# Kernel tuning notes

Measured on AMD Instinct MI355X. Metric: run time of the kernel, lower is better.

## Reference

```python
import jax, jax.numpy as jnp
import numpy as np

DECAY = 0.99
EPS = 1e-05


def setup_inputs() -> dict:
    key = jax.random.key(0)
    k1, k2 = jax.random.split(key)
    B, C, H, W = 64, 256, 32, 32
    n_embed = 1024
    inp = jax.random.normal(k1, (B, C, H, W), dtype=jnp.float32)
    embed = jax.random.normal(k2, (C, n_embed), dtype=jnp.float32)
    cluster_size = jnp.ones((n_embed,), dtype=jnp.float32)
    embed_avg = embed.copy()
    return {"input": inp, "embed": embed, "cluster_size": cluster_size, "embed_avg": embed_avg}


def reference(input, embed, cluster_size, embed_avg):
    n_embed = embed.shape[1]
    x = jnp.transpose(input, (0, 2, 3, 1))            # B,H,W,C
    flatten = x.reshape(-1, x.shape[-1])              # N,C
    dist = ((flatten ** 2).sum(1, keepdims=True)
            - 2.0 * flatten @ embed
            + (embed ** 2).sum(0, keepdims=True))     # N,n_embed
    embed_ind = jnp.argmin(dist, axis=1)              # N
    quantize = jnp.take(embed.T, embed_ind, axis=0).reshape(x.shape)  # B,H,W,C
    embed_ind_out = embed_ind.reshape(x.shape[:-1])   # B,H,W

    # EMA codebook update (training=True)
    onehot_sum = jnp.zeros((n_embed,), dtype=flatten.dtype).at[embed_ind].add(1.0)
    embed_sum = jax.ops.segment_sum(flatten, embed_ind, num_segments=n_embed).T  # C,n_embed
    cluster_size_new = cluster_size * DECAY + onehot_sum * (1.0 - DECAY)
    embed_avg_new = embed_avg * DECAY + embed_sum * (1.0 - DECAY)
    n = cluster_size_new.sum()
    cs = (cluster_size_new + EPS) / (n + n_embed * EPS) * n
    embed_new = embed_avg_new / cs[None, :]

    diff = jax.lax.stop_gradient(quantize) - x
    quantize_st = x + jax.lax.stop_gradient(quantize - x)   # straight-through
    quantize_out = jnp.transpose(quantize_st, (0, 3, 1, 2)) # B,C,H,W
    return quantize_out, diff, embed_ind_out, embed_new, cluster_size_new, embed_avg_new
```

## Files before the change

kernel.cpp:

```cpp
#include <hip/hip_runtime.h>
#include <cstddef>

static constexpr int OUT_DIFF = 16777216;
static constexpr int OUT_IDX  = 33554432;
static constexpr int OUT_ENEW = 33619968;
static constexpr int OUT_CSN  = 33882112;
static constexpr int OUT_EAVG = 33883136;

__global__ __launch_bounds__(256) void k_prep(const float* __restrict__ embed,
                                              const float* __restrict__ cs_in,
                                              float* __restrict__ embedT,
                                              float* __restrict__ esq,
                                              float* __restrict__ nval) {
  const int wg = blockIdx.x;
  const int tid = threadIdx.x;
  if (wg < 1024) {
    __shared__ float col[256];
    const int k = wg;
    float v = embed[(size_t)tid * 1024 + k];
    col[tid] = v;
    embedT[(size_t)k * 256 + tid] = v;
    __syncthreads();
    if (tid == 0) {
#pragma clang fp contract(off)
      float s = 0.f;
      for (int c = 0; c < 256; ++c) { float u = col[c]; s += u * u; }
      esq[k] = s;
    }
  } else {
    __shared__ float red[256];
    float v = cs_in[tid] + cs_in[tid + 256] + cs_in[tid + 512] + cs_in[tid + 768];
    red[tid] = v;
    __syncthreads();
    for (int off = 128; off > 0; off >>= 1) {
      if (tid < off) red[tid] += red[tid + off];
      __syncthreads();
    }
    if (tid == 0) nval[0] = 0.99f * red[0] + 0.01f * 65536.0f;
  }
}

__global__ __launch_bounds__(256) void k_flatten(const float* __restrict__ inp,
                                                 float* __restrict__ flat) {
  const int tid = threadIdx.x;
  const int b = blockIdx.x >> 4;
  const int hw0 = (blockIdx.x & 15) * 64;
  __shared__ float t[64 * 257];
#pragma unroll
  for (int r = 0; r < 16; ++r) {
    int i = tid + r * 256;
    int c = i >> 4, l = i & 15;
    float4 v = *(const float4*)(inp + (size_t)b * 262144 + (size_t)c * 1024 + hw0 + l * 4);
    t[(l * 4 + 0) * 257 + c] = v.x;
    t[(l * 4 + 1) * 257 + c] = v.y;
    t[(l * 4 + 2) * 257 + c] = v.z;
    t[(l * 4 + 3) * 257 + c] = v.w;
  }
  __syncthreads();
#pragma unroll
  for (int r = 0; r < 16; ++r) {
    int i = tid + r * 256;
    int hw = i >> 6, c4 = (i & 63) * 4;
    float4 o;
    o.x = t[hw * 257 + c4 + 0];
    o.y = t[hw * 257 + c4 + 1];
    o.z = t[hw * 257 + c4 + 2];
    o.w = t[hw * 257 + c4 + 3];
    *(float4*)(flat + ((size_t)(b * 1024 + hw0 + hw)) * 256 + c4) = o;
  }
}

__global__ __launch_bounds__(256) void k_argmin(const float* __restrict__ inp,
                                                const float* __restrict__ embed,
                                                const float* __restrict__ esq,
                                                int* __restrict__ idx_out,
                                                float* __restrict__ idxf_out) {
  __shared__ float xs[8][128];
  __shared__ float es[8][256];
  __shared__ float xsqh[2][128];
  __shared__ float xsq_s[128];

  const int tid = threadIdx.x;
  const int n0 = blockIdx.x * 128;
  const int b = n0 >> 10;
  const int hw0 = n0 & 1023;
  const float* xbase = inp + (size_t)b * 262144 + hw0;

  {
#pragma clang fp contract(off)
    const int p = tid & 127, h = tid >> 7;
    const float* xb = xbase + (size_t)(h * 128) * 1024 + p;
    float r[8];
#pragma unroll
    for (int j = 0; j < 8; ++j) { float v = xb[(size_t)j * 1024]; r[j] = v * v; }
#pragma unroll 1
    for (int blk = 1; blk < 16; ++blk) {
#pragma unroll
      for (int j = 0; j < 8; ++j) { float v = xb[(size_t)(blk * 8 + j) * 1024]; r[j] += v * v; }
    }
    xsqh[h][p] = ((r[0] + r[1]) + (r[2] + r[3])) + ((r[4] + r[5]) + (r[6] + r[7]));
    __syncthreads();
    if (tid < 128) xsq_s[tid] = xsqh[0][tid] + xsqh[1][tid];
  }

  const int tc = tid & 15, tr = tid >> 4;
  float bestv[8];
  int besti[8];
#pragma unroll
  for (int p = 0; p < 8; ++p) { bestv[p] = 3.0e38f; besti[p] = 0; }

#pragma unroll 1
  for (int kt = 0; kt < 4; ++kt) {
    const int k0 = kt * 256;
    float acc[8][16];
#pragma unroll
    for (int p = 0; p < 8; ++p)
#pragma unroll
      for (int j = 0; j < 16; ++j) acc[p][j] = 0.f;

#pragma unroll 1
    for (int cs = 0; cs < 32; ++cs) {
      const int c0 = cs * 8;
      {
        int cc = tid >> 5, l = tid & 31;
        *(float4*)&xs[cc][l * 4] =
            *(const float4*)(xbase + (size_t)(c0 + cc) * 1024 + l * 4);
      }
#pragma unroll
      for (int j = 0; j < 2; ++j) {
        int i = tid + j * 256;
        int cc = i >> 6, l = i & 63;
        *(float4*)&es[cc][l * 4] =
            *(const float4*)(embed + (size_t)(c0 + cc) * 1024 + k0 + l * 4);
      }
      __syncthreads();
#pragma unroll
      for (int cc = 0; cc < 8; ++cc) {
        alignas(16) float xr[8];
        alignas(16) float er[16];
        *(float4*)&xr[0] = *(float4*)&xs[cc][tr * 8];
        *(float4*)&xr[4] = *(float4*)&xs[cc][tr * 8 + 4];
#pragma unroll
        for (int g = 0; g < 4; ++g)
          *(float4*)&er[g * 4] = *(float4*)&es[cc][g * 64 + tc * 4];
#pragma unroll
        for (int p = 0; p < 8; ++p)
#pragma unroll
          for (int j = 0; j < 16; ++j)
            acc[p][j] = __builtin_fmaf(xr[p], er[j], acc[p][j]);
      }
      __syncthreads();
    }
    alignas(16) float esqr[16];
#pragma unroll
    for (int g = 0; g < 4; ++g)
      *(float4*)&esqr[g * 4] = *(const float4*)(esq + k0 + g * 64 + tc * 4);
#pragma unroll
    for (int p = 0; p < 8; ++p) {
      float xq = xsq_s[tr * 8 + p];
#pragma unroll
      for (int g = 0; g < 4; ++g)
#pragma unroll
        for (int jj = 0; jj < 4; ++jj) {
          int j = g * 4 + jj;
          float d = (xq - 2.0f * acc[p][j]) + esqr[j];
          int k = k0 + g * 64 + tc * 4 + jj;
          if (d < bestv[p]) { bestv[p] = d; besti[p] = k; }
        }
    }
  }
#pragma unroll
  for (int p = 0; p < 8; ++p) {
    float v = bestv[p];
    int ii = besti[p];
#pragma unroll
    for (int off = 1; off < 16; off <<= 1) {
      float ov = __shfl_xor(v, off);
      int oi = __shfl_xor(ii, off);
      if (ov < v || (ov == v && oi < ii)) { v = ov; ii = oi; }
    }
    if (tc == 0) {
      int n = n0 + tr * 8 + p;
      idx_out[n] = ii;
      idxf_out[n] = (float)ii;
    }
  }
}

__global__ __launch_bounds__(256) void k_update(const int* __restrict__ idx,
                                                const float* __restrict__ flat,
                                                const float* __restrict__ cs_in,
                                                const float* __restrict__ eavg,
                                                const float* __restrict__ nval,
                                                float* __restrict__ csn_out,
                                                float* __restrict__ eavgn_out,
                                                float* __restrict__ enew_out) {
  const int k = blockIdx.x;
  const int tid = threadIdx.x;
  const int w = tid >> 6, lane = tid & 63;
  __shared__ int list_s[8192];
  __shared__ int lcnt;
  __shared__ float sums_s[4][256];
  float4 acc = make_float4(0.f, 0.f, 0.f, 0.f);
  int total = 0;
#pragma unroll 1
  for (int seg = 0; seg < 65536; seg += 8192) {
    __syncthreads();
    if (tid == 0) lcnt = 0;
    __syncthreads();
#pragma unroll 1
    for (int r = 0; r < 32; ++r) {
      int i = seg + r * 256 + tid;
      if (idx[i] == k) { int pos = atomicAdd(&lcnt, 1); list_s[pos] = i; }
    }
    __syncthreads();
    int cnt = lcnt;
    total += cnt;
#pragma unroll 1
    for (int e = w; e < cnt; e += 4) {
      const float* row = flat + (size_t)list_s[e] * 256;
      float4 x4 = *(const float4*)(row + lane * 4);
      acc.x += x4.x; acc.y += x4.y; acc.z += x4.z; acc.w += x4.w;
    }
  }
  __syncthreads();
  *(float4*)&sums_s[w][lane * 4] = acc;
  __syncthreads();
  {
    const int c = tid;
    float s = ((sums_s[0][c] + sums_s[1][c]) + sums_s[2][c]) + sums_s[3][c];
    float cntf = (float)total;
    float csn = cs_in[k] * 0.99f + cntf * 0.01f;
    float nv = nval[0];
    float csk = (csn + 1e-5f) / (nv + 0.01024f) * nv;
    float ean = eavg[(size_t)c * 1024 + k] * 0.99f + s * 0.01f;
    eavgn_out[(size_t)c * 1024 + k] = ean;
    enew_out[(size_t)c * 1024 + k] = ean / csk;
    if (tid == 0) csn_out[k] = csn;
  }
}

__global__ __launch_bounds__(256) void k_diffq(const int* __restrict__ idx,
                                               const float* __restrict__ embedT,
                                               float* __restrict__ flat_diff,
                                               float* __restrict__ q_out) {
  const int tid = threadIdx.x;
  const int b = blockIdx.x >> 4;
  const int hw0 = (blockIdx.x & 15) * 64;
  const int n0 = b * 1024 + hw0;
  __shared__ float t[64 * 257];
#pragma unroll
  for (int r = 0; r < 16; ++r) {
    int i = tid + r * 256;
    int hw = i >> 6, c4 = (i & 63) * 4;
    int n = n0 + hw;
    int kk = idx[n];
    float4 q = *(const float4*)(embedT + (size_t)kk * 256 + c4);
    float4 x = *(const float4*)(flat_diff + (size_t)n * 256 + c4);
    float4 d;
    d.x = q.x - x.x; d.y = q.y - x.y; d.z = q.z - x.z; d.w = q.w - x.w;
    *(float4*)(flat_diff + (size_t)n * 256 + c4) = d;
    t[hw * 257 + c4 + 0] = x.x + d.x;
    t[hw * 257 + c4 + 1] = x.y + d.y;
    t[hw * 257 + c4 + 2] = x.z + d.z;
    t[hw * 257 + c4 + 3] = x.w + d.w;
  }
  __syncthreads();
#pragma unroll
  for (int r = 0; r < 16; ++r) {
    int i = tid + r * 256;
    int c = i >> 4, l = i & 15;
    float4 o;
    o.x = t[(l * 4 + 0) * 257 + c];
    o.y = t[(l * 4 + 1) * 257 + c];
    o.z = t[(l * 4 + 2) * 257 + c];
    o.w = t[(l * 4 + 3) * 257 + c];
    *(float4*)(q_out + (size_t)b * 262144 + (size_t)c * 1024 + hw0 + l * 4) = o;
  }
}

extern "C" void kernel_launch(void* const* d_in, const int* in_sizes, int n_in,
                              void* d_out, int out_size, void* d_ws, size_t ws_size,
                              hipStream_t stream) {
  (void)in_sizes; (void)n_in; (void)out_size; (void)ws_size;
  const float* inp   = (const float*)d_in[0];
  const float* embed = (const float*)d_in[1];
  const float* cs_in = (const float*)d_in[2];
  const float* eavg  = (const float*)d_in[3];
  float* out = (float*)d_out;

  int*   idx_ws = (int*)d_ws;
  float* wsf    = (float*)d_ws;
  float* embedT = wsf + 65536;
  float* esq    = embedT + 262144;
  float* nval   = esq + 1024;

  hipLaunchKernelGGL(k_prep,    dim3(1025), dim3(256), 0, stream, embed, cs_in, embedT, esq, nval);
  hipLaunchKernelGGL(k_flatten, dim3(1024), dim3(256), 0, stream, inp, out + OUT_DIFF);
  hipLaunchKernelGGL(k_argmin,  dim3(512),  dim3(256), 0, stream, inp, embed, esq, idx_ws, out + OUT_IDX);
  hipLaunchKernelGGL(k_update,  dim3(1024), dim3(256), 0, stream, idx_ws, out + OUT_DIFF, cs_in, eavg, nval,
                     out + OUT_CSN, out + OUT_EAVG, out + OUT_ENEW);
  hipLaunchKernelGGL(k_diffq,   dim3(1024), dim3(256), 0, stream, idx_ws, embedT, out + OUT_DIFF, out);
}
```

Measured before the change: 963.3 us.

## Replace per-code full index scan with counting-sort buckets and double-buffered argmin loads

The EMA update previously had each of 1024 blocks scan all 65536 indices, so total index traffic grew with codes times points. Now argmin counts assignments atomically, a single-block scan computes offsets, a scatter kernel builds per-code buckets, and k_update sums only its own rows. A separate transposing kernel applies the EMA. The argmin inner loop also double-buffers its LDS tiles with direct global-to-LDS loads, and the prep kernel transposes the codebook with tiles. This adds more kernel launches and a serial single-block scan, and the bucket order makes summation order nondeterministic.

```diff
diff --git a/kernel.cpp b/kernel.cpp
--- a/kernel.cpp
+++ b/kernel.cpp
@@ -7,36 +7,53 @@
 static constexpr int OUT_CSN  = 33882112;
 static constexpr int OUT_EAVG = 33883136;
 
+__device__ __forceinline__ void gll16(const float* g, float* l) {
+  __builtin_amdgcn_global_load_lds((const __attribute__((address_space(1))) void*)g,
+                                   (__attribute__((address_space(3))) void*)l, 16, 0, 0);
+}
+
 __global__ __launch_bounds__(256) void k_prep(const float* __restrict__ embed,
-                                              const float* __restrict__ cs_in,
                                               float* __restrict__ embedT,
                                               float* __restrict__ esq,
-                                              float* __restrict__ nval) {
+                                              int* __restrict__ cnt) {
   const int wg = blockIdx.x;
   const int tid = threadIdx.x;
-  if (wg < 1024) {
-    __shared__ float col[256];
-    const int k = wg;
-    float v = embed[(size_t)tid * 1024 + k];
-    col[tid] = v;
-    embedT[(size_t)k * 256 + tid] = v;
-    __syncthreads();
-    if (tid == 0) {
+  if (wg < 64) {
+    __shared__ float tt[64 * 65];
+    const int k0 = (wg >> 2) * 64, c0 = (wg & 3) * 64;
+#pragma unroll
+    for (int r = 0; r < 4; ++r) {
+      int i = tid + r * 256;
+      int cc = i >> 4, kL = (i & 15) * 4;
+      float4 v = *(const float4*)(embed + (size_t)(c0 + cc) * 1024 + k0 + kL);
+      tt[(kL + 0) * 65 + cc] = v.x;
+      tt[(kL + 1) * 65 + cc] = v.y;
+      tt[(kL + 2) * 65 + cc] = v.z;
+      tt[(kL + 3) * 65 + cc] = v.w;
+    }
+    __syncthreads();
+#pragma unroll
+    for (int r = 0; r < 4; ++r) {
+      int i = tid + r * 256;
+      int kk = i >> 4, cL = (i & 15) * 4;
+      float4 o;
+      o.x = tt[kk * 65 + cL + 0];
+      o.y = tt[kk * 65 + cL + 1];
+      o.z = tt[kk * 65 + cL + 2];
+      o.w = tt[kk * 65 + cL + 3];
+      *(float4*)(embedT + (size_t)(k0 + kk) * 256 + c0 + cL) = o;
+    }
+  } else if (wg < 68) {
+    const int k = (wg - 64) * 256 + tid;
+    {
 #pragma clang fp contract(off)
       float s = 0.f;
-      for (int c = 0; c < 256; ++c) { float u = col[c]; s += u * u; }
+#pragma unroll 1
+      for (int c = 0; c < 256; ++c) { float u = embed[(size_t)c * 1024 + k]; s += u * u; }
       esq[k] = s;
     }
   } else {
-    __shared__ float red[256];
-    float v = cs_in[tid] + cs_in[tid + 256] + cs_in[tid + 512] + cs_in[tid + 768];
-    red[tid] = v;
-    __syncthreads();
-    for (int off = 128; off > 0; off >>= 1) {
-      if (tid < off) red[tid] += red[tid + off];
-      __syncthreads();
-    }
-    if (tid == 0) nval[0] = 0.99f * red[0] + 0.01f * 65536.0f;
+    ((int4*)cnt)[tid] = make_int4(0, 0, 0, 0);
   }
 }
 
@@ -74,13 +91,16 @@
                                                 const float* __restrict__ embed,
                                                 const float* __restrict__ esq,
                                                 int* __restrict__ idx_out,
-                                                float* __restrict__ idxf_out) {
-  __shared__ float xs[8][128];
-  __shared__ float es[8][256];
+                                                float* __restrict__ idxf_out,
+                                                int* __restrict__ cnt) {
+  __shared__ float xs[2][8][128];
+  __shared__ float es[2][8][256];
   __shared__ float xsqh[2][128];
   __shared__ float xsq_s[128];
 
   const int tid = threadIdx.x;
+  const int lane = tid & 63;
+  const int w = tid >> 6;
   const int n0 = blockIdx.x * 128;
   const int b = n0 >> 10;
   const int hw0 = n0 & 1023;
@@ -109,6 +129,16 @@
 #pragma unroll
   for (int p = 0; p < 8; ++p) { bestv[p] = 3.0e38f; besti[p] = 0; }
 
+#define STAGE(buf, c0)                                                               \
+  do {                                                                               \
+    gll16(xbase + (size_t)((c0) + 2 * w + (lane >> 5)) * 1024 + (lane & 31) * 4,     \
+          &xs[buf][0][0] + w * 256);                                                 \
+    gll16(embed + (size_t)((c0) + w) * 1024 + k0 + lane * 4,                         \
+          &es[buf][0][0] + w * 256);                                                 \
+    gll16(embed + (size_t)((c0) + 4 + w) * 1024 + k0 + lane * 4,                     \
+          &es[buf][0][0] + (4 + w) * 256);                                           \
+  } while (0)
+
 #pragma unroll 1
   for (int kt = 0; kt < 4; ++kt) {
     const int k0 = kt * 256;
@@ -118,31 +148,22 @@
 #pragma unroll
       for (int j = 0; j < 16; ++j) acc[p][j] = 0.f;
 
+    STAGE(0, 0);
+    __syncthreads();
+
 #pragma unroll 1
     for (int cs = 0; cs < 32; ++cs) {
-      const int c0 = cs * 8;
-      {
-        int cc = tid >> 5, l = tid & 31;
-        *(float4*)&xs[cc][l * 4] =
-            *(const float4*)(xbase + (size_t)(c0 + cc) * 1024 + l * 4);
-      }
-#pragma unroll
-      for (int j = 0; j < 2; ++j) {
-        int i = tid + j * 256;
-        int cc = i >> 6, l = i & 63;
-        *(float4*)&es[cc][l * 4] =
-            *(const float4*)(embed + (size_t)(c0 + cc) * 1024 + k0 + l * 4);
-      }
-      __syncthreads();
+      const int cur = cs & 1;
+      if (cs < 31) STAGE(cur ^ 1, (cs + 1) * 8);
 #pragma unroll
       for (int cc = 0; cc < 8; ++cc) {
         alignas(16) float xr[8];
         alignas(16) float er[16];
-        *(float4*)&xr[0] = *(float4*)&xs[cc][tr * 8];
-        *(float4*)&xr[4] = *(float4*)&xs[cc][tr * 8 + 4];
+        *(float4*)&xr[0] = *(float4*)&xs[cur][cc][tr * 8];
+        *(float4*)&xr[4] = *(float4*)&xs[cur][cc][tr * 8 + 4];
 #pragma unroll
         for (int g = 0; g < 4; ++g)
-          *(float4*)&er[g * 4] = *(float4*)&es[cc][g * 64 + tc * 4];
+          *(float4*)&er[g * 4] = *(float4*)&es[cur][cc][g * 64 + tc * 4];
 #pragma unroll
         for (int p = 0; p < 8; ++p)
 #pragma unroll
@@ -151,6 +172,7 @@
       }
       __syncthreads();
     }
+
     alignas(16) float esqr[16];
 #pragma unroll
     for (int g = 0; g < 4; ++g)
@@ -169,6 +191,8 @@
         }
     }
   }
+#undef STAGE
+
 #pragma unroll
   for (int p = 0; p < 8; ++p) {
     float v = bestv[p];
@@ -183,60 +207,121 @@
       int n = n0 + tr * 8 + p;
       idx_out[n] = ii;
       idxf_out[n] = (float)ii;
-    }
-  }
-}
-
-__global__ __launch_bounds__(256) void k_update(const int* __restrict__ idx,
+      atomicAdd(cnt + ii, 1);
+    }
+  }
+}
+
+__global__ __launch_bounds__(1024) void k_scan(const int* __restrict__ cnt,
+                                               const float* __restrict__ cs_in,
+                                               int* __restrict__ offs,
+                                               int* __restrict__ cursor,
+                                               float* __restrict__ csn_out,
+                                               float* __restrict__ nval) {
+  __shared__ int sc[1024];
+  __shared__ float red[1024];
+  const int tid = threadIdx.x;
+  const int c = cnt[tid];
+  const float csv = cs_in[tid];
+  sc[tid] = c;
+  red[tid] = csv;
+  __syncthreads();
+#pragma unroll 1
+  for (int off = 1; off < 1024; off <<= 1) {
+    int v = sc[tid];
+    int add = (tid >= off) ? sc[tid - off] : 0;
+    __syncthreads();
+    sc[tid] = v + add;
+    __syncthreads();
+  }
+  const int incl = sc[tid];
+  const int start = incl - c;
+  offs[tid] = start;
+  cursor[tid] = start;
+  if (tid == 1023) offs[1024] = incl;
+  csn_out[tid] = csv * 0.99f + (float)c * 0.01f;
+#pragma unroll 1
+  for (int off = 512; off > 0; off >>= 1) {
+    if (tid < off) red[tid] += red[tid + off];
+    __syncthreads();
+  }
+  if (tid == 0) nval[0] = 0.99f * red[0] + 0.01f * 65536.0f;
+}
+
+__global__ __launch_bounds__(256) void k_scatter(const int* __restrict__ idx,
+                                                 int* __restrict__ cursor,
+                                                 int* __restrict__ bucket) {
+  const int n = blockIdx.x * 256 + threadIdx.x;
+  const int k = idx[n];
+  const int pos = atomicAdd(cursor + k, 1);
+  bucket[pos] = n;
+}
+
+__global__ __launch_bounds__(256) void k_update(const int* __restrict__ offs,
+                                                const int* __restrict__ bucket,
                                                 const float* __restrict__ flat,
-                                                const float* __restrict__ cs_in,
-                                                const float* __restrict__ eavg,
-                                                const float* __restrict__ nval,
-                                                float* __restrict__ csn_out,
-                                                float* __restrict__ eavgn_out,
-                                                float* __restrict__ enew_out) {
+                                                float* __restrict__ sums) {
   const int k = blockIdx.x;
   const int tid = threadIdx.x;
   const int w = tid >> 6, lane = tid & 63;
-  __shared__ int list_s[8192];
-  __shared__ int lcnt;
   __shared__ float sums_s[4][256];
+  const int start = offs[k], end = offs[k + 1];
   float4 acc = make_float4(0.f, 0.f, 0.f, 0.f);
-  int total = 0;
-#pragma unroll 1
-  for (int seg = 0; seg < 65536; seg += 8192) {
-    __syncthreads();
-    if (tid == 0) lcnt = 0;
-    __syncthreads();
-#pragma unroll 1
-    for (int r = 0; r < 32; ++r) {
-      int i = seg + r * 256 + tid;
-      if (idx[i] == k) { int pos = atomicAdd(&lcnt, 1); list_s[pos] = i; }
-    }
-    __syncthreads();
-    int cnt = lcnt;
-    total += cnt;
-#pragma unroll 1
-    for (int e = w; e < cnt; e += 4) {
-      const float* row = flat + (size_t)list_s[e] * 256;
-      float4 x4 = *(const float4*)(row + lane * 4);
-      acc.x += x4.x; acc.y += x4.y; acc.z += x4.z; acc.w += x4.w;
-    }
-  }
-  __syncthreads();
+#pragma unroll 1
+  for (int e = start + w; e < end; e += 4) {
+    const float* row = flat + (size_t)bucket[e] * 256;
+    float4 x4 = *(const float4*)(row + lane * 4);
+    acc.x += x4.x; acc.y += x4.y; acc.z += x4.z; acc.w += x4.w;
+  }
   *(float4*)&sums_s[w][lane * 4] = acc;
   __syncthreads();
-  {
-    const int c = tid;
-    float s = ((sums_s[0][c] + sums_s[1][c]) + sums_s[2][c]) + sums_s[3][c];
-    float cntf = (float)total;
-    float csn = cs_in[k] * 0.99f + cntf * 0.01f;
+  const float s = ((sums_s[0][tid] + sums_s[1][tid]) + sums_s[2][tid]) + sums_s[3][tid];
+  sums[(size_t)k * 256 + tid] = s;
+}
+
+__global__ __launch_bounds__(256) void k_ema(const float* __restrict__ sums,
+                                             const float* __restrict__ eavg,
+                                             const float* __restrict__ csn,
+                                             const float* __restrict__ nval,
+                                             float* __restrict__ eavgn,
+                                             float* __restrict__ enew) {
+  __shared__ float t[64 * 65];
+  __shared__ float csks[64];
+  const int tid = threadIdx.x;
+  const int k0 = (blockIdx.x >> 2) * 64, c0 = (blockIdx.x & 3) * 64;
+  if (tid < 64) {
     float nv = nval[0];
-    float csk = (csn + 1e-5f) / (nv + 0.01024f) * nv;
-    float ean = eavg[(size_t)c * 1024 + k] * 0.99f + s * 0.01f;
-    eavgn_out[(size_t)c * 1024 + k] = ean;
-    enew_out[(size_t)c * 1024 + k] = ean / csk;
-    if (tid == 0) csn_out[k] = csn;
+    float cv = csn[k0 + tid];
+    csks[tid] = (cv + 1e-5f) / (nv + 0.01024f) * nv;
+  }
+#pragma unroll
+  for (int r = 0; r < 4; ++r) {
+    int i = tid + r * 256;
+    int kk = i >> 4, cL = (i & 15) * 4;
+    float4 v = *(const float4*)(sums + (size_t)(k0 + kk) * 256 + c0 + cL);
+    t[(cL + 0) * 65 + kk] = v.x;
+    t[(cL + 1) * 65 + kk] = v.y;
+    t[(cL + 2) * 65 + kk] = v.z;
+    t[(cL + 3) * 65 + kk] = v.w;
+  }
+  __syncthreads();
+#pragma unroll
+  for (int r = 0; r < 4; ++r) {
+    int i = tid + r * 256;
+    int c = i >> 4, kL = (i & 15) * 4;
+    size_t o = (size_t)(c0 + c) * 1024 + k0 + kL;
+    float4 ev = *(const float4*)(eavg + o);
+    float4 ean, en;
+    ean.x = ev.x * 0.99f + t[c * 65 + kL + 0] * 0.01f;
+    ean.y = ev.y * 0.99f + t[c * 65 + kL + 1] * 0.01f;
+    ean.z = ev.z * 0.99f + t[c * 65 + kL + 2] * 0.01f;
+    ean.w = ev.w * 0.99f + t[c * 65 + kL + 3] * 0.01f;
+    en.x = ean.x / csks[kL + 0];
+    en.y = ean.y / csks[kL + 1];
+    en.z = ean.z / csks[kL + 2];
+    en.w = ean.w / csks[kL + 3];
+    *(float4*)(eavgn + o) = ean;
+    *(float4*)(enew + o) = en;
   }
 }
 
@@ -290,15 +375,27 @@
   float* out = (float*)d_out;
 
   int*   idx_ws = (int*)d_ws;
+  int*   bucket = idx_ws + 65536;
+  int*   cnt    = bucket + 65536;
+  int*   offs   = cnt + 1024;
+  int*   cursor = offs + 1536;
   float* wsf    = (float*)d_ws;
-  float* embedT = wsf + 65536;
-  float* esq    = embedT + 262144;
-  float* nval   = esq + 1024;
-
-  hipLaunchKernelGGL(k_prep,    dim3(1025), dim3(256), 0, stream, embed, cs_in, embedT, esq, nval);
-  hipLaunchKernelGGL(k_flatten, dim3(1024), dim3(256), 0, stream, inp, out + OUT_DIFF);
-  hipLaunchKernelGGL(k_argmin,  dim3(512),  dim3(256), 0, stream, inp, embed, esq, idx_ws, out + OUT_IDX);
-  hipLaunchKernelGGL(k_update,  dim3(1024), dim3(256), 0, stream, idx_ws, out + OUT_DIFF, cs_in, eavg, nval,
-                     out + OUT_CSN, out + OUT_EAVG, out + OUT_ENEW);
-  hipLaunchKernelGGL(k_diffq,   dim3(1024), dim3(256), 0, stream, idx_ws, embedT, out + OUT_DIFF, out);
-}
+  float* nval   = wsf + 136192;
+  float* esq    = wsf + 136448;
+  float* sums   = wsf + 137472;
+  float* embedT = wsf + 399616;
+
+  float* flat = out + OUT_DIFF;
+
+  hipLaunchKernelGGL(k_prep,    dim3(69),   dim3(256),  0, stream, embed, embedT, esq, cnt);
+  hipLaunchKernelGGL(k_flatten, dim3(1024), dim3(256),  0, stream, inp, flat);
+  hipLaunchKernelGGL(k_argmin,  dim3(512),  dim3(256),  0, stream, inp, embed, esq,
+                     idx_ws, out + OUT_IDX, cnt);
+  hipLaunchKernelGGL(k_scan,    dim3(1),    dim3(1024), 0, stream, cnt, cs_in, offs, cursor,
+                     out + OUT_CSN, nval);
+  hipLaunchKernelGGL(k_scatter, dim3(256),  dim3(256),  0, stream, idx_ws, cursor, bucket);
+  hipLaunchKernelGGL(k_update,  dim3(1024), dim3(256),  0, stream, offs, bucket, flat, sums);
+  hipLaunchKernelGGL(k_ema,     dim3(64),   dim3(256),  0, stream, sums, eavg, out + OUT_CSN,
+                     nval, out + OUT_EAVG, out + OUT_ENEW);
+  hipLaunchKernelGGL(k_diffq,   dim3(1024), dim3(256),  0, stream, idx_ws, embedT, flat, out);
+}
```

Result: slower. 1.093 ms (+13.5%).
